# Optimization experiments

Hardware: AMD Instinct MI355X
Metric: run time of the kernel (lower is better)

Reference implementation:

```python
import jax, jax.numpy as jnp
import numpy as np

DIM = 512
HEADS = 8
NUM_KEYS = 256
TOPK = 32
DIM_HEAD = 128
LN_EPS = 1e-5


def setup_inputs() -> dict:
    key = jax.random.key(0)
    k1, k2, k3, k4 = jax.random.split(key, 4)
    b, t = 2, 1024
    dim_query = DIM_HEAD * HEADS * 2
    x = jax.random.normal(k1, (b, t, DIM), dtype=jnp.float32)
    # nn.Linear(dim, dim_query, bias=False): weight (dim_query, dim), default kaiming-ish; use scaled normal
    Wq = jax.random.normal(k2, (dim_query, DIM), dtype=jnp.float32) / np.sqrt(DIM)
    # keys: (heads, num_keys, 2, dim_head), std = 1/sqrt(dim_head)
    keys = jax.random.normal(k3, (HEADS, NUM_KEYS, 2, DIM_HEAD), dtype=jnp.float32) / np.sqrt(DIM_HEAD)
    # values: (num_keys**2, dim), std = 1/sqrt(dim)
    values = jax.random.normal(k4, (NUM_KEYS ** 2, DIM), dtype=jnp.float32) / np.sqrt(DIM)
    ln_gamma = jnp.ones((DIM_HEAD,), dtype=jnp.float32)
    ln_beta = jnp.zeros((DIM_HEAD,), dtype=jnp.float32)
    return {"x": x, "Wq": Wq, "keys": keys, "values": values,
            "ln_gamma": ln_gamma, "ln_beta": ln_beta}


def reference(x, Wq, keys, values, ln_gamma, ln_beta):
    b, t, _ = x.shape
    h, n, _, d = keys.shape  # (heads, num_keys, 2, dim_head)
    k = TOPK

    # queries: 'b t (p h d)' -> (b, t, 2, h, d)
    q = jnp.einsum('btc,qc->btq', x, Wq).reshape(b, t, 2, h, d)

    # LayerNorm over dim_head (use_layernorm=True path)
    mu = q.mean(axis=-1, keepdims=True)
    var = q.var(axis=-1, keepdims=True)
    q = (q - mu) * jax.lax.rsqrt(var + LN_EPS) * ln_gamma + ln_beta

    # dots: 'p b t h d, h n p d -> b t h p n'
    dots = jnp.einsum('btphd,hnpd->bthpn', q, keys)

    # top-k per sub-key half: (b, t, h, 2, k)
    scores, indices = jax.lax.top_k(dots, k)
    sx, sy = scores[..., 0, :], scores[..., 1, :]
    ix, iy = indices[..., 0, :], indices[..., 1, :]

    # outer combination -> (b, t, h, k*k)
    all_scores = (sx[..., :, None] + sy[..., None, :]).reshape(b, t, h, k * k)
    all_indices = (ix[..., :, None] * n + iy[..., None, :]).reshape(b, t, h, k * k)

    final_scores, final_idx = jax.lax.top_k(all_scores, k)  # (b, t, h, k)
    value_indices = jnp.take_along_axis(all_indices, final_idx, axis=-1)
    attn = jax.nn.softmax(final_scores, axis=-1)

    vi = value_indices.reshape(b * t, h * k)
    w = attn.reshape(b * t, h * k)

    # EmbeddingBag(mode='sum') with per-sample weights
    gathered = values[vi]                      # (bt, hk, dim)
    out = jnp.einsum('nkd,nk->nd', gathered, w)
    return out.reshape(b, t, -1)
```

## Files before the change

### kernel.cpp

```cpp
#include <hip/hip_runtime.h>
#include <math.h>

#define DQ 2048
#define CDIM 512
#define NKEYS 256
#define KSEL 32

__device__ __forceinline__ bool rank_before(float as, int ai, float bs, int bi) {
  return (as > bs) || (as == bs && ai < bi);
}
static __device__ __forceinline__ float bf2f(unsigned int u) {
  union { unsigned int i; float f; } v; v.i = u << 16; return v.f;
}
static __device__ __forceinline__ unsigned int f2bf(float f) {
  union { float f; unsigned int i; } v; v.f = f;
  unsigned int r = v.i + 0x7fffu + ((v.i >> 16) & 1u);
  return r >> 16;
}

__global__ __launch_bounds__(256) void qgemm_ln(
    const float* __restrict__ X, const float* __restrict__ W,
    const float* __restrict__ gamma, const float* __restrict__ beta,
    float* __restrict__ Q) {
  __shared__ float As[16 * 68];
  __shared__ float Bs[16 * 132];
  const int tid = threadIdx.x;
  const int m0 = blockIdx.x * 64, n0 = blockIdx.y * 128;
  const int tx = tid & 15, ty = tid >> 4;
  const int am = tid >> 2, ak = (tid & 3) * 4;
  const int bn = tid >> 1, bk = (tid & 1) * 8;
  float acc[4][8] = {};
  float4 av  = *(const float4*)&X[(size_t)(m0 + am) * CDIM + ak];
  float4 bv0 = *(const float4*)&W[(size_t)(n0 + bn) * CDIM + bk];
  float4 bv1 = *(const float4*)&W[(size_t)(n0 + bn) * CDIM + bk + 4];
  for (int kt = 0; kt < CDIM; kt += 16) {
    __syncthreads();
    As[(ak + 0) * 68 + am] = av.x; As[(ak + 1) * 68 + am] = av.y;
    As[(ak + 2) * 68 + am] = av.z; As[(ak + 3) * 68 + am] = av.w;
    Bs[(bk + 0) * 132 + bn] = bv0.x; Bs[(bk + 1) * 132 + bn] = bv0.y;
    Bs[(bk + 2) * 132 + bn] = bv0.z; Bs[(bk + 3) * 132 + bn] = bv0.w;
    Bs[(bk + 4) * 132 + bn] = bv1.x; Bs[(bk + 5) * 132 + bn] = bv1.y;
    Bs[(bk + 6) * 132 + bn] = bv1.z; Bs[(bk + 7) * 132 + bn] = bv1.w;
    __syncthreads();
    if (kt + 16 < CDIM) {
      av  = *(const float4*)&X[(size_t)(m0 + am) * CDIM + kt + 16 + ak];
      bv0 = *(const float4*)&W[(size_t)(n0 + bn) * CDIM + kt + 16 + bk];
      bv1 = *(const float4*)&W[(size_t)(n0 + bn) * CDIM + kt + 16 + bk + 4];
    }
    #pragma unroll
    for (int kk = 0; kk < 16; ++kk) {
      float4 a4  = *(const float4*)&As[kk * 68 + ty * 4];
      float4 b4a = *(const float4*)&Bs[kk * 132 + tx * 8];
      float4 b4b = *(const float4*)&Bs[kk * 132 + tx * 8 + 4];
      const float ar[4] = {a4.x, a4.y, a4.z, a4.w};
      const float br[8] = {b4a.x, b4a.y, b4a.z, b4a.w, b4b.x, b4b.y, b4b.z, b4b.w};
      #pragma unroll
      for (int i = 0; i < 4; ++i)
        #pragma unroll
        for (int j = 0; j < 8; ++j)
          acc[i][j] += ar[i] * br[j];
    }
  }
  float g[8], bta[8];
  #pragma unroll
  for (int j = 0; j < 8; ++j) { g[j] = gamma[tx * 8 + j]; bta[j] = beta[tx * 8 + j]; }
  #pragma unroll
  for (int i = 0; i < 4; ++i) {
    float s = 0.f, sq = 0.f;
    #pragma unroll
    for (int j = 0; j < 8; ++j) { s += acc[i][j]; sq += acc[i][j] * acc[i][j]; }
    #pragma unroll
    for (int m = 1; m < 16; m <<= 1) {
      s += __shfl_xor(s, m, 64);
      sq += __shfl_xor(sq, m, 64);
    }
    float mean = s * (1.0f / 128.0f);
    float var = sq * (1.0f / 128.0f) - mean * mean;
    float rs = 1.0f / sqrtf(var + 1e-5f);
    float o[8];
    #pragma unroll
    for (int j = 0; j < 8; ++j) o[j] = (acc[i][j] - mean) * rs * g[j] + bta[j];
    float* dst = &Q[(size_t)(m0 + ty * 4 + i) * DQ + n0 + tx * 8];
    *(float4*)dst = make_float4(o[0], o[1], o[2], o[3]);
    *(float4*)(dst + 4) = make_float4(o[4], o[5], o[6], o[7]);
  }
}

__global__ __launch_bounds__(256) void transpose_keys(
    const float* __restrict__ keys, float* __restrict__ keysT) {
  __shared__ float tile[64 * 129];
  const int hp = blockIdx.x, h = hp >> 1, p = hp & 1;
  const int n0 = blockIdx.y * 64;
  {
    const int n = threadIdx.x >> 2;
    const int d0 = (threadIdx.x & 3) * 32;
    const float* src = &keys[(((size_t)h * NKEYS + n0 + n) * 2 + p) * 128 + d0];
    #pragma unroll
    for (int j = 0; j < 32; j += 4) {
      float4 v = *(const float4*)(src + j);
      tile[n * 129 + d0 + j + 0] = v.x;
      tile[n * 129 + d0 + j + 1] = v.y;
      tile[n * 129 + d0 + j + 2] = v.z;
      tile[n * 129 + d0 + j + 3] = v.w;
    }
  }
  __syncthreads();
  {
    const int d = threadIdx.x >> 1;
    const int nh = (threadIdx.x & 1) * 32;
    float* dst = &keysT[((size_t)hp * 128 + d) * NKEYS + n0 + nh];
    #pragma unroll
    for (int j = 0; j < 32; j += 4) {
      float4 o = make_float4(tile[(nh + j + 0) * 129 + d], tile[(nh + j + 1) * 129 + d],
                             tile[(nh + j + 2) * 129 + d], tile[(nh + j + 3) * 129 + d]);
      *(float4*)(dst + j) = o;
    }
  }
}

__global__ __launch_bounds__(512, 5) void dots_sel(
    const float* __restrict__ Q, const float* __restrict__ keysT,
    float* __restrict__ s1s, int* __restrict__ s1i) {
  const int hp = blockIdx.x;
  const int chunk = blockIdx.y;
  const int h = hp >> 1, p = hp & 1;
  const int t0 = chunk * 32;
  const int tid = threadIdx.x;
  const int w = tid >> 6, lane = tid & 63;
  const int wu = __builtin_amdgcn_readfirstlane(w);
  const float* q0 = &Q[(size_t)(t0 + wu * 4 + 0) * DQ + p * 1024 + h * 128];
  const float* q1 = q0 + DQ;
  const float* q2 = q0 + 2 * DQ;
  const float* q3 = q0 + 3 * DQ;
  const float* kT = keysT + (size_t)hp * 128 * NKEYS + lane * 4;
  float acc[4][4] = {};
  #pragma unroll 2
  for (int kt = 0; kt < 128; kt += 4) {
    float4 a0 = *(const float4*)&q0[kt];
    float4 a1 = *(const float4*)&q1[kt];
    float4 a2 = *(const float4*)&q2[kt];
    float4 a3 = *(const float4*)&q3[kt];
    const float a0r[4] = {a0.x, a0.y, a0.z, a0.w};
    const float a1r[4] = {a1.x, a1.y, a1.z, a1.w};
    const float a2r[4] = {a2.x, a2.y, a2.z, a2.w};
    const float a3r[4] = {a3.x, a3.y, a3.z, a3.w};
    #pragma unroll
    for (int kk = 0; kk < 4; ++kk) {
      float4 b4 = *(const float4*)&kT[(size_t)(kt + kk) * NKEYS];
      const float br[4] = {b4.x, b4.y, b4.z, b4.w};
      #pragma unroll
      for (int j = 0; j < 4; ++j) {
        acc[0][j] += a0r[kk] * br[j];
        acc[1][j] += a1r[kk] * br[j];
        acc[2][j] += a2r[kk] * br[j];
        acc[3][j] += a3r[kk] * br[j];
      }
    }
  }
  #define CE1(S, I, a, b, dd)                                                  \
    {                                                                          \
      bool sw_ = (dd) ? rank_before(S[a], I[a], S[b], I[b])                    \
                      : rank_before(S[b], I[b], S[a], I[a]);                   \
      if (sw_) {                                                               \
        float ts_ = S[a]; S[a] = S[b]; S[b] = ts_;                             \
        int ti_ = I[a]; I[a] = I[b]; I[b] = ti_;                               \
      }                                                                        \
    }
  #define CEP(a, b, dd) { CE1(sA, iA, a, b, dd) CE1(sB, iB, a, b, dd) }
  #define CROSSP(L, dd)                                                        \
    {                                                                          \
      bool amHigh = (lane & (L)) != 0;                                         \
      bool flip = amHigh != (dd);                                              \
      _Pragma("unroll")                                                        \
      for (int r = 0; r < 4; ++r) {                                            \
        float osA = __shfl_xor(sA[r], (L), 64);                                \
        int oiA = __shfl_xor(iA[r], (L), 64);                                  \
        float osB = __shfl_xor(sB[r], (L), 64);                                \
        int oiB = __shfl_xor(iB[r], (L), 64);                                  \
        bool tA = rank_before(osA, oiA, sA[r], iA[r]) != flip;                 \
        if (tA) { sA[r] = osA; iA[r] = oiA; }                                  \
        bool tB = rank_before(osB, oiB, sB[r], iB[r]) != flip;                 \
        if (tB) { sB[r] = osB; iB[r] = oiB; }                                  \
      }                                                                        \
    }
  #pragma unroll
  for (int ii = 0; ii < 4; ii += 2) {
    float sA[4], sB[4]; int iA[4], iB[4];
    #pragma unroll
    for (int r = 0; r < 4; ++r) {
      sA[r] = acc[ii][r];     iA[r] = lane * 4 + r;
      sB[r] = acc[ii + 1][r]; iB[r] = lane * 4 + r;
    }
    CEP(0, 1, false); CEP(2, 3, true);
    {
      bool dd = (lane & 1) != 0;
      CEP(0, 2, dd); CEP(1, 3, dd); CEP(0, 1, dd); CEP(2, 3, dd);
    }
    #pragma unroll
    for (int K = 8; K <= 256; K <<= 1) {
      bool dd = (lane & (K >> 2)) != 0;
      #pragma unroll
      for (int L = K >> 3; L >= 1; L >>= 1) CROSSP(L, dd);
      CEP(0, 2, dd); CEP(1, 3, dd); CEP(0, 1, dd); CEP(2, 3, dd);
    }
    const int instA = (t0 + w * 4 + ii) * 16 + hp;
    const int instB = instA + 16;
    if (lane < 8) {
      *(float4*)&s1s[(size_t)instA * KSEL + lane * 4] = make_float4(sA[0], sA[1], sA[2], sA[3]);
      *(int4*)&s1i[(size_t)instA * KSEL + lane * 4] = make_int4(iA[0], iA[1], iA[2], iA[3]);
      *(float4*)&s1s[(size_t)instB * KSEL + lane * 4] = make_float4(sB[0], sB[1], sB[2], sB[3]);
      *(int4*)&s1i[(size_t)instB * KSEL + lane * 4] = make_int4(iB[0], iB[1], iB[2], iB[3]);
    }
  }
  #undef CE1
  #undef CEP
  #undef CROSSP
}

__constant__ unsigned short slot_ij[128] = {
  0,1,2,3,4,5,6,7,8,9,10,11,12,13,14,15,16,17,18,19,20,21,22,23,24,25,26,27,28,29,30,31,
  32,33,34,35,36,37,38,39,40,41,42,43,44,45,46,47,
  64,65,66,67,68,69,70,71,72,73,
  96,97,98,99,100,101,102,103,
  128,129,130,131,132,133,
  160,161,162,163,164,
  192,193,194,195,
  224,225,226,227,
  256,257,258,
  288,289,290,
  320,321, 352,353, 384,385, 416,417, 448,449, 480,481,
  512,544,576,608,640,672,704,736,768,800,832,864,896,928,960,992,
  0xFFFF,0xFFFF,0xFFFF,0xFFFF,0xFFFF,0xFFFF,0xFFFF,0xFFFF,0xFFFF
};

__global__ __launch_bounds__(256) void stage2_kernel(
    const float* __restrict__ s1s, const int* __restrict__ s1i,
    float* __restrict__ wgt, int* __restrict__ vidx) {
  const int th = blockIdx.x * 4 + (threadIdx.x >> 6);
  const int lane = threadIdx.x & 63;
  const int bx = th * 64;
  const int by = bx + 32;
  float s[2]; int id[2];
  #pragma unroll
  for (int r = 0; r < 2; ++r) {
    int sl = slot_ij[lane * 2 + r];
    if (sl != 0xFFFF) {
      s[r] = s1s[bx + (sl >> 5)] + s1s[by + (sl & 31)];
      id[r] = sl;
    } else {
      s[r] = -INFINITY; id[r] = 0x7fffffff;
    }
  }
  #define CE2(dd)                                                              \
    {                                                                          \
      bool sw = (dd) ? rank_before(s[0], id[0], s[1], id[1])                   \
                     : rank_before(s[1], id[1], s[0], id[0]);                  \
      if (sw) {                                                                \
        float ts = s[0]; s[0] = s[1]; s[1] = ts;                               \
        int ti = id[0]; id[0] = id[1]; id[1] = ti;                             \
      }                                                                        \
    }
  #define CROSS2(L, dd)                                                        \
    {                                                                          \
      bool amHigh = (lane & (L)) != 0;                                         \
      bool flip = amHigh != (dd);                                              \
      _Pragma("unroll")                                                        \
      for (int r = 0; r < 2; ++r) {                                            \
        float os = __shfl_xor(s[r], (L), 64);                                  \
        int oi = __shfl_xor(id[r], (L), 64);                                   \
        bool take = rank_before(os, oi, s[r], id[r]) != flip;                  \
        if (take) { s[r] = os; id[r] = oi; }                                   \
      }                                                                        \
    }
  { bool dd = (lane & 1) != 0; CE2(dd); }
  #pragma unroll
  for (int K = 4; K <= 128; K <<= 1) {
    bool dd = (lane & (K >> 1)) != 0;
    #pragma unroll
    for (int L = K >> 2; L >= 1; L >>= 1) CROSS2(L, dd);
    CE2(dd);
  }
  #undef CE2
  #undef CROSS2
  float smax = __shfl(s[0], 0, 64);
  float e0 = 0.f, e1 = 0.f;
  if (lane < 16) { e0 = expf(s[0] - smax); e1 = expf(s[1] - smax); }
  float part = e0 + e1;
  #pragma unroll
  for (int m = 1; m < 16; m <<= 1) part += __shfl_xor(part, m, 64);
  if (lane < 16) {
    int f0 = id[0], f1 = id[1];
    int vi0 = s1i[bx + (f0 >> 5)] * NKEYS + s1i[by + (f0 & 31)];
    int vi1 = s1i[bx + (f1 >> 5)] * NKEYS + s1i[by + (f1 & 31)];
    wgt[(size_t)th * KSEL + lane * 2] = e0 / part;
    wgt[(size_t)th * KSEL + lane * 2 + 1] = e1 / part;
    vidx[(size_t)th * KSEL + lane * 2] = vi0;
    vidx[(size_t)th * KSEL + lane * 2 + 1] = vi1;
  }
}

__global__ __launch_bounds__(256) void convert_values(
    const float* __restrict__ values, unsigned int* __restrict__ vbf) {
  const size_t g = ((size_t)blockIdx.x * 256 + threadIdx.x) * 8;
  float4 a = *(const float4*)(values + g);
  float4 b = *(const float4*)(values + g + 4);
  uint4 pk;
  pk.x = f2bf(a.x) | (f2bf(a.y) << 16);
  pk.y = f2bf(a.z) | (f2bf(a.w) << 16);
  pk.z = f2bf(b.x) | (f2bf(b.y) << 16);
  pk.w = f2bf(b.z) | (f2bf(b.w) << 16);
  *(uint4*)(vbf + g / 2) = pk;
}

__global__ __launch_bounds__(256) void gather_bf16(
    const float* __restrict__ wgt, const int* __restrict__ vidx,
    const unsigned short* __restrict__ vbf, float* __restrict__ out) {
  const int t = blockIdx.x;
  const int tid = threadIdx.x, w = tid >> 6, lane = tid & 63;
  __shared__ float ws_[256];
  __shared__ int vs_[256];
  __shared__ float part[4 * 520];
  ws_[tid] = wgt[(size_t)t * 256 + tid];
  vs_[tid] = vidx[(size_t)t * 256 + tid];
  __syncthreads();
  float acc[8] = {};
  const int c0 = lane * 8;
  #pragma unroll 1
  for (int phase = 0; phase < 4; ++phase) {
    for (int e = w; e < 256; e += 4) {
      const int row = vs_[e];
      if ((row >> 14) != phase) continue;
      const float wv = ws_[e];
      uint4 pk = *(const uint4*)(vbf + (size_t)row * CDIM + c0);
      acc[0] += wv * bf2f(pk.x & 0xffff); acc[1] += wv * bf2f(pk.x >> 16);
      acc[2] += wv * bf2f(pk.y & 0xffff); acc[3] += wv * bf2f(pk.y >> 16);
      acc[4] += wv * bf2f(pk.z & 0xffff); acc[5] += wv * bf2f(pk.z >> 16);
      acc[6] += wv * bf2f(pk.w & 0xffff); acc[7] += wv * bf2f(pk.w >> 16);
    }
  }
  #pragma unroll
  for (int j = 0; j < 8; j += 4)
    *(float4*)&part[w * 520 + c0 + j] =
        make_float4(acc[j], acc[j + 1], acc[j + 2], acc[j + 3]);
  __syncthreads();
  const int c2 = tid * 2;
  float r0 = part[c2] + part[520 + c2] + part[1040 + c2] + part[1560 + c2];
  float r1 = part[c2 + 1] + part[520 + c2 + 1] + part[1040 + c2 + 1] + part[1560 + c2 + 1];
  *(float2*)(out + (size_t)t * CDIM + c2) = make_float2(r0, r1);
}

__global__ __launch_bounds__(256) void gather_kernel(
    const float* __restrict__ wgt, const int* __restrict__ vidx,
    const float* __restrict__ values, float* __restrict__ out) {
  const int tp = blockIdx.x;
  const int tid = threadIdx.x;
  __shared__ float ws_[512];
  __shared__ int vs_[512];
  ws_[tid] = wgt[(size_t)tp * 512 + tid];
  ws_[tid + 256] = wgt[(size_t)tp * 512 + tid + 256];
  vs_[tid] = vidx[(size_t)tp * 512 + tid];
  vs_[tid + 256] = vidx[(size_t)tp * 512 + tid + 256];
  __syncthreads();
  const int sub = tid >> 7;
  const int c4 = (tid & 127) * 4;
  const float* wp = &ws_[sub * 256];
  const int* vp = &vs_[sub * 256];
  float4 a = make_float4(0.f, 0.f, 0.f, 0.f);
  #pragma unroll 4
  for (int e = 0; e < 256; ++e) {
    float4 vv = *(const float4*)(values + (size_t)vp[e] * CDIM + c4);
    float wv = wp[e];
    a.x += wv * vv.x; a.y += wv * vv.y; a.z += wv * vv.z; a.w += wv * vv.w;
  }
  *(float4*)(out + (size_t)(tp * 2 + sub) * CDIM + c4) = a;
}

extern "C" void kernel_launch(void* const* d_in, const int* in_sizes, int n_in,
                              void* d_out, int out_size, void* d_ws, size_t ws_size,
                              hipStream_t stream) {
  const float* X      = (const float*)d_in[0];
  const float* W      = (const float*)d_in[1];
  const float* keys   = (const float*)d_in[2];
  const float* values = (const float*)d_in[3];
  const float* gamma  = (const float*)d_in[4];
  const float* beta   = (const float*)d_in[5];
  char* ws = (char*)d_ws;
  float* s1s = (float*)(ws);
  int*   s1i = (int*)  (ws + (4u << 20));
  float* wgt = (float*)(ws + (8u << 20));
  int*   vix = (int*)  (ws + (10u << 20));
  float* Q   = (float*)(ws + (12u << 20));
  float* kT  = (float*)(ws + (28u << 20));
  unsigned int* vbf = (unsigned int*)(ws + (12u << 20));

  const bool bf16_path = ws_size >= (76u << 20);

  transpose_keys<<<dim3(16, 4), 256, 0, stream>>>(keys, kT);
  qgemm_ln<<<dim3(32, 16), 256, 0, stream>>>(X, W, gamma, beta, Q);
  dots_sel<<<dim3(16, 64), 512, 0, stream>>>(Q, kT, s1s, s1i);
  stage2_kernel<<<4096, 256, 0, stream>>>(s1s, s1i, wgt, vix);
  if (bf16_path) {
    convert_values<<<16384, 256, 0, stream>>>(values, vbf);
    gather_bf16<<<2048, 256, 0, stream>>>(wgt, vix, (const unsigned short*)vbf, (float*)d_out);
  } else {
    gather_kernel<<<1024, 256, 0, stream>>>(wgt, vix, values, (float*)d_out);
  }
}
```

Measured before the change: 439.8 us.

## Sort order-preserving uint keys only and recover top-k indices via ballots

The stage-1 top-k bitonic sort now runs on scores mapped to order-preserving unsigned integers, without carrying indices, and processes all four query rows together. This halves the shuffle traffic and simplifies the compare-exchange to plain min/max. Indices of the 32 selected scores are then recovered by matching each sorted value against the original scores with wave ballots, handling ties in lane order. This adds 32 serial readlane/ballot steps per row and relies on tie handling matching the reference ordering.

```diff
diff --git a/kernel.cpp b/kernel.cpp
--- a/kernel.cpp
+++ b/kernel.cpp
@@ -16,6 +16,14 @@
   union { float f; unsigned int i; } v; v.f = f;
   unsigned int r = v.i + 0x7fffu + ((v.i >> 16) & 1u);
   return r >> 16;
+}
+static __device__ __forceinline__ unsigned int f2ord(float f) {
+  unsigned int b = __float_as_uint(f);
+  return b ^ (unsigned int)(((int)b >> 31) | (int)0x80000000);
+}
+static __device__ __forceinline__ float ord2f(unsigned int u) {
+  unsigned int b = u ^ (unsigned int)(((int)(~u) >> 31) | (int)0x80000000);
+  return __uint_as_float(b);
 }
 
 __global__ __launch_bounds__(256) void qgemm_ln(
@@ -157,64 +165,94 @@
       }
     }
   }
-  #define CE1(S, I, a, b, dd)                                                  \
+  unsigned int ts[4][4], tso[4][4];
+  #pragma unroll
+  for (int t = 0; t < 4; ++t)
+    #pragma unroll
+    for (int r = 0; r < 4; ++r) {
+      unsigned int b = f2ord(acc[t][r]);
+      ts[t][r] = b; tso[t][r] = b;
+    }
+
+  #define CES(a, b, dd)                                                        \
     {                                                                          \
-      bool sw_ = (dd) ? rank_before(S[a], I[a], S[b], I[b])                    \
-                      : rank_before(S[b], I[b], S[a], I[a]);                   \
-      if (sw_) {                                                               \
-        float ts_ = S[a]; S[a] = S[b]; S[b] = ts_;                             \
-        int ti_ = I[a]; I[a] = I[b]; I[b] = ti_;                               \
+      _Pragma("unroll")                                                        \
+      for (int t_ = 0; t_ < 4; ++t_) {                                         \
+        unsigned int x_ = ts[t_][a], y_ = ts[t_][b];                           \
+        unsigned int lo_ = x_ < y_ ? x_ : y_;                                  \
+        unsigned int hi_ = x_ < y_ ? y_ : x_;                                  \
+        ts[t_][a] = (dd) ? lo_ : hi_;                                          \
+        ts[t_][b] = (dd) ? hi_ : lo_;                                          \
       }                                                                        \
     }
-  #define CEP(a, b, dd) { CE1(sA, iA, a, b, dd) CE1(sB, iB, a, b, dd) }
-  #define CROSSP(L, dd)                                                        \
+  #define XRS(L, dd)                                                           \
     {                                                                          \
-      bool amHigh = (lane & (L)) != 0;                                         \
-      bool flip = amHigh != (dd);                                              \
+      const bool flip_ = (((lane & (L)) != 0) != (dd));                        \
       _Pragma("unroll")                                                        \
-      for (int r = 0; r < 4; ++r) {                                            \
-        float osA = __shfl_xor(sA[r], (L), 64);                                \
-        int oiA = __shfl_xor(iA[r], (L), 64);                                  \
-        float osB = __shfl_xor(sB[r], (L), 64);                                \
-        int oiB = __shfl_xor(iB[r], (L), 64);                                  \
-        bool tA = rank_before(osA, oiA, sA[r], iA[r]) != flip;                 \
-        if (tA) { sA[r] = osA; iA[r] = oiA; }                                  \
-        bool tB = rank_before(osB, oiB, sB[r], iB[r]) != flip;                 \
-        if (tB) { sB[r] = osB; iB[r] = oiB; }                                  \
-      }                                                                        \
-    }
-  #pragma unroll
-  for (int ii = 0; ii < 4; ii += 2) {
-    float sA[4], sB[4]; int iA[4], iB[4];
-    #pragma unroll
-    for (int r = 0; r < 4; ++r) {
-      sA[r] = acc[ii][r];     iA[r] = lane * 4 + r;
-      sB[r] = acc[ii + 1][r]; iB[r] = lane * 4 + r;
-    }
-    CEP(0, 1, false); CEP(2, 3, true);
-    {
-      bool dd = (lane & 1) != 0;
-      CEP(0, 2, dd); CEP(1, 3, dd); CEP(0, 1, dd); CEP(2, 3, dd);
-    }
-    #pragma unroll
-    for (int K = 8; K <= 256; K <<= 1) {
-      bool dd = (lane & (K >> 2)) != 0;
-      #pragma unroll
-      for (int L = K >> 3; L >= 1; L >>= 1) CROSSP(L, dd);
-      CEP(0, 2, dd); CEP(1, 3, dd); CEP(0, 1, dd); CEP(2, 3, dd);
-    }
-    const int instA = (t0 + w * 4 + ii) * 16 + hp;
-    const int instB = instA + 16;
+      for (int t_ = 0; t_ < 4; ++t_)                                           \
+        _Pragma("unroll")                                                      \
+        for (int r_ = 0; r_ < 4; ++r_) {                                       \
+          unsigned int o_ = __shfl_xor(ts[t_][r_], (L), 64);                   \
+          bool take_ = ((o_ > ts[t_][r_]) != flip_);                           \
+          if (take_) ts[t_][r_] = o_;                                          \
+        }                                                                      \
+    }
+  CES(0, 1, false); CES(2, 3, true);
+  {
+    bool dd = (lane & 1) != 0;
+    CES(0, 2, dd); CES(1, 3, dd); CES(0, 1, dd); CES(2, 3, dd);
+  }
+  #pragma unroll
+  for (int K = 8; K <= 256; K <<= 1) {
+    bool dd = (lane & (K >> 2)) != 0;
+    #pragma unroll
+    for (int L = K >> 3; L >= 1; L >>= 1) XRS(L, dd);
+    CES(0, 2, dd); CES(1, 3, dd); CES(0, 1, dd); CES(2, 3, dd);
+  }
+  #undef CES
+  #undef XRS
+
+  #pragma unroll
+  for (int t = 0; t < 4; ++t) {
+    unsigned long long us0 = 0, us1 = 0, us2 = 0, us3 = 0;
+    unsigned int prevw = 0u;
+    int id0 = 0, id1 = 0, id2 = 0, id3 = 0;
+    #pragma unroll
+    for (int j = 0; j < 32; ++j) {
+      unsigned int tw;
+      if ((j & 3) == 0)      tw = (unsigned int)__builtin_amdgcn_readlane((int)ts[t][0], j >> 2);
+      else if ((j & 3) == 1) tw = (unsigned int)__builtin_amdgcn_readlane((int)ts[t][1], j >> 2);
+      else if ((j & 3) == 2) tw = (unsigned int)__builtin_amdgcn_readlane((int)ts[t][2], j >> 2);
+      else                   tw = (unsigned int)__builtin_amdgcn_readlane((int)ts[t][3], j >> 2);
+      const bool same = (j != 0) && (tw == prevw);
+      us0 = same ? us0 : 0ull; us1 = same ? us1 : 0ull;
+      us2 = same ? us2 : 0ull; us3 = same ? us3 : 0ull;
+      unsigned long long b0 = __ballot(tso[t][0] == tw) & ~us0;
+      unsigned long long b1 = __ballot(tso[t][1] == tw) & ~us1;
+      unsigned long long b2 = __ballot(tso[t][2] == tw) & ~us2;
+      unsigned long long b3 = __ballot(tso[t][3] == tw) & ~us3;
+      unsigned long long mu = b0 | b1 | b2 | b3;
+      const int Lw = __ffsll((unsigned long long)mu) - 1;
+      const unsigned long long bit = 1ull << Lw;
+      const int rr = (b0 & bit) ? 0 : (b1 & bit) ? 1 : (b2 & bit) ? 2 : 3;
+      us0 |= (rr == 0) ? bit : 0ull; us1 |= (rr == 1) ? bit : 0ull;
+      us2 |= (rr == 2) ? bit : 0ull; us3 |= (rr == 3) ? bit : 0ull;
+      const int idj = (Lw << 2) | rr;
+      if (lane == (j >> 2)) {
+        if ((j & 3) == 0)      id0 = idj;
+        else if ((j & 3) == 1) id1 = idj;
+        else if ((j & 3) == 2) id2 = idj;
+        else                   id3 = idj;
+      }
+      prevw = tw;
+    }
     if (lane < 8) {
-      *(float4*)&s1s[(size_t)instA * KSEL + lane * 4] = make_float4(sA[0], sA[1], sA[2], sA[3]);
-      *(int4*)&s1i[(size_t)instA * KSEL + lane * 4] = make_int4(iA[0], iA[1], iA[2], iA[3]);
-      *(float4*)&s1s[(size_t)instB * KSEL + lane * 4] = make_float4(sB[0], sB[1], sB[2], sB[3]);
-      *(int4*)&s1i[(size_t)instB * KSEL + lane * 4] = make_int4(iB[0], iB[1], iB[2], iB[3]);
-    }
-  }
-  #undef CE1
-  #undef CEP
-  #undef CROSSP
+      const int inst = (t0 + w * 4 + t) * 16 + hp;
+      *(float4*)&s1s[(size_t)inst * KSEL + lane * 4] =
+          make_float4(ord2f(ts[t][0]), ord2f(ts[t][1]), ord2f(ts[t][2]), ord2f(ts[t][3]));
+      *(int4*)&s1i[(size_t)inst * KSEL + lane * 4] = make_int4(id0, id1, id2, id3);
+    }
+  }
 }
 
 __constant__ unsigned short slot_ij[128] = {
```

Measured after the change: 471.8 us. 1.07x slower.
